# Performance work log

Hardware: AMD Instinct MI355X
Metric: run time of the kernel (lower is better)

The kernel has to match this reference:

```python
import jax, jax.numpy as jnp
import numpy as np
from jax import lax

THRESHOLDS = (0.25, 0.5, 0.75)
TAU = 100.0
NUM_CLASSES = 10
K = 32
RES_Z = 5.0
# each of the 16 binary logic gates is bilinear: g(a,b) = c0 + c1*a + c2*b + c3*a*b
GATE_COEF = jnp.array([
    [0, 0, 0, 0],   # 0: False
    [0, 0, 0, 1],   # 1: a AND b
    [0, 1, 0, -1],  # 2: a AND NOT b
    [0, 1, 0, 0],   # 3: a  (residual gate)
    [0, 0, 1, -1],  # 4: NOT a AND b
    [0, 0, 1, 0],   # 5: b
    [0, 1, 1, -2],  # 6: XOR
    [0, 1, 1, -1],  # 7: OR
    [1, -1, -1, 1], # 8: NOR
    [1, -1, -1, 2], # 9: XNOR
    [1, 0, -1, 0],  # 10: NOT b
    [1, 0, -1, 1],  # 11: a OR NOT b
    [1, -1, 0, 0],  # 12: NOT a
    [1, -1, 0, 1],  # 13: NOT a OR b
    [1, 0, 0, -1],  # 14: NAND
    [1, 0, 0, 0],   # 15: True
], dtype=jnp.float32)


def _gate_logits(key, shape):
    # residual init: pass-through gate (id 3) dominates
    w = 0.01 * jax.random.normal(key, shape, dtype=jnp.float32)
    return w.at[..., 3].add(RES_Z)


def _leaf_idx(rng, C, O, leaves=8, cpt=2, kk=9):
    # each tree uses cpt random input channels; each leaf picks one of them and a 3x3 position
    ch2 = rng.integers(0, C, size=(O, cpt))
    sel = rng.integers(0, cpt, size=(O, leaves))
    ch = np.take_along_axis(ch2, sel, axis=1)
    pos = rng.integers(0, kk, size=(O, leaves))
    return jnp.asarray(ch * kk + pos, dtype=jnp.int32)


def setup_inputs() -> dict:
    key = jax.random.key(0)
    ks = jax.random.split(key, 9)
    rng = np.random.default_rng(0)
    B = 128
    d = {"x": jax.random.uniform(ks[0], (B, 3, 32, 32), dtype=jnp.float32)}
    in_chs = [3 * len(THRESHOLDS), K, 4 * K, 16 * K]
    out_chs = [K, 4 * K, 16 * K, 32 * K]
    for i, (ci, co) in enumerate(zip(in_chs, out_chs)):
        d[f"c{i+1}_idx"] = _leaf_idx(rng, ci, co)
        d[f"c{i+1}_w"] = _gate_logits(ks[1 + i], (co, 7, 16))
    dims = [32 * K * 4, 1280 * K, 640 * K, 320 * K]
    for i in range(3):
        di, do = dims[i], dims[i + 1]
        d[f"l{i+1}_a"] = jnp.asarray(rng.integers(0, di, size=(do,)), dtype=jnp.int32)
        d[f"l{i+1}_b"] = jnp.asarray(rng.integers(0, di, size=(do,)), dtype=jnp.int32)
        d[f"l{i+1}_w"] = _gate_logits(ks[5 + i], (do, 16))
    return d


def _mix(logits):
    # softmax over 16 gates folded into 4 bilinear coefficients (fused gate mixture)
    return jax.nn.softmax(logits, axis=-1) @ GATE_COEF


def binarize(x):
    return jnp.concatenate([(x > t).astype(x.dtype) for t in THRESHOLDS], axis=1)


def tree_conv(x, leaf_idx, logits):
    # x: (B,C,H,W); leaf_idx: (O,8) into C*9 channel-major patch; logits: (O,7,16)
    B, C, H, W = x.shape
    xp = jnp.pad(x, ((0, 0), (0, 0), (1, 1), (1, 1)))
    patches = jnp.stack([xp[:, :, i:i + H, j:j + W] for i in range(3) for j in range(3)], axis=2)
    patches = patches.reshape(B, C * 9, H, W)
    vals = patches[:, leaf_idx]  # (B,O,8,H,W)
    m = _mix(logits)             # (O,7,4)
    node = 0
    for lvl in (4, 2, 1):
        a, b = vals[:, :, 0::2], vals[:, :, 1::2]
        w = m[:, node:node + lvl]  # (O,lvl,4)
        w0 = w[..., 0][None, :, :, None, None]
        w1 = w[..., 1][None, :, :, None, None]
        w2 = w[..., 2][None, :, :, None, None]
        w3 = w[..., 3][None, :, :, None, None]
        vals = w0 + w1 * a + w2 * b + w3 * (a * b)
        node += lvl
    return vals[:, :, 0]  # (B,O,H,W)


def or_pool(x):
    # OR of relaxed binary values == max pool 2x2/2
    return lax.reduce_window(x, -jnp.inf, lax.max, (1, 1, 2, 2), (1, 1, 2, 2), "VALID")


def logic_layer(x, a_idx, b_idx, logits):
    a = x[:, a_idx]  # (B,O)
    b = x[:, b_idx]
    w = _mix(logits)  # (O,4)
    return w[:, 0] + w[:, 1] * a + w[:, 2] * b + w[:, 3] * (a * b)


def group_sum(x):
    B = x.shape[0]
    return x.reshape(B, NUM_CLASSES, -1).sum(axis=-1) / TAU


def reference(x, c1_idx, c1_w, c2_idx, c2_w, c3_idx, c3_w, c4_idx, c4_w,
              l1_a, l1_b, l1_w, l2_a, l2_b, l2_w, l3_a, l3_b, l3_w):
    h = binarize(x)
    h = or_pool(tree_conv(h, c1_idx, c1_w))
    h = or_pool(tree_conv(h, c2_idx, c2_w))
    h = or_pool(tree_conv(h, c3_idx, c3_w))
    h = or_pool(tree_conv(h, c4_idx, c4_w))
    h = h.reshape(h.shape[0], -1)  # (B, 4096)
    h = logic_layer(h, l1_a, l1_b, l1_w)
    h = logic_layer(h, l2_a, l2_b, l2_w)
    h = logic_layer(h, l3_a, l3_b, l3_w)
    return group_sum(h)  # (B, 10)
```

## Files before the change

### kernel.cpp

```cpp
#include <hip/hip_runtime.h>

#define BATCH 128

__device__ __constant__ float GC[16][4] = {
  {0,0,0,0},{0,0,0,1},{0,1,0,-1},{0,1,0,0},
  {0,0,1,-1},{0,0,1,0},{0,1,1,-2},{0,1,1,-1},
  {1,-1,-1,1},{1,-1,-1,2},{1,0,-1,0},{1,0,-1,1},
  {1,-1,0,0},{1,-1,0,1},{1,0,0,-1},{1,0,0,0}};

struct MixArgs {
  const float* logits[7];
  float* out[7];
  int n[7];
};

__global__ __launch_bounds__(256) void mix_kernel(MixArgs args, int total) {
  int gid = blockIdx.x * 256 + threadIdx.x;
  if (gid >= total) return;
  int g = gid;
  int seg = 0;
  while (seg < 6 && g >= args.n[seg]) { g -= args.n[seg]; ++seg; }
  const float* lp = args.logits[seg] + (size_t)g * 16;
  float* op = args.out[seg] + (size_t)g * 4;

  float e[16];
  float s = 0.f;
  #pragma unroll
  for (int i = 0; i < 16; ++i) { e[i] = __expf(lp[i]); s += e[i]; }
  float inv = 1.0f / s;
  float w0 = 0.f, w1 = 0.f, w2 = 0.f, w3 = 0.f;
  #pragma unroll
  for (int i = 0; i < 16; ++i) {
    float p = e[i] * inv;
    w0 = fmaf(p, GC[i][0], w0);
    w1 = fmaf(p, GC[i][1], w1);
    w2 = fmaf(p, GC[i][2], w2);
    w3 = fmaf(p, GC[i][3], w3);
  }
  op[0] = w0; op[1] = w1; op[2] = w2; op[3] = w3;
}

__global__ __launch_bounds__(256) void transpose_x(
    const float* __restrict__ x, float* __restrict__ xt) {
  __shared__ float tile[64 * 129];
  int c    = blockIdx.x;
  int pix0 = blockIdx.y * 64;
  {
    int pix = threadIdx.x & 63;
    int b0  = threadIdx.x >> 6;
    #pragma unroll 4
    for (int i = 0; i < 32; ++i) {
      int b = b0 + i * 4;
      tile[pix * 129 + b] = x[((size_t)(b * 3 + c) * 1024) + pix0 + pix];
    }
  }
  __syncthreads();
  {
    int b     = threadIdx.x & 127;
    int pix0i = threadIdx.x >> 7;
    #pragma unroll 4
    for (int i = 0; i < 32; ++i) {
      int pix = pix0i + i * 2;
      xt[(size_t)(c * 1024 + pix0 + pix) * BATCH + b] = tile[pix * 129 + b];
    }
  }
}

__device__ __forceinline__ float2 gate2(float2 a, float2 b, float4 w) {
  float2 r;
  r.x = fmaf(w.w, a.x * b.x, fmaf(w.z, b.x, fmaf(w.y, a.x, w.x)));
  r.y = fmaf(w.w, a.y * b.y, fmaf(w.z, b.y, fmaf(w.y, a.y, w.x)));
  return r;
}

template <int C, int H, int W, int O, bool BIN>
__global__ __launch_bounds__(256) void tree_conv_pool_t(
    const float* __restrict__ in_t, const int* __restrict__ leaf_idx,
    const float* __restrict__ m, float* __restrict__ out_t) {
  constexpr int PH = H / 2, PW = W / 2, PIX = PH * PW;

  int wave = threadIdx.x >> 6;
  int b2   = threadIdx.x & 63;
  int q = blockIdx.x * 4 + wave;
  int o = q / PIX;
  int p = q - o * PIX;
  int ph = p / PW;
  int pw = p - ph * PW;

  int4 liA = ((const int4*)(leaf_idx + o * 8))[0];
  int4 liB = ((const int4*)(leaf_idx + o * 8))[1];
  int li[8] = {liA.x, liA.y, liA.z, liA.w, liB.x, liB.y, liB.z, liB.w};
  const float4* mw = (const float4*)(m + o * 28);

  float2 v[4][8];
  #pragma unroll
  for (int l = 0; l < 8; ++l) {
    int idx = li[l];
    int c = idx / 9;
    int k = idx - c * 9;
    int di = k / 3 - 1;
    int dj = (k % 3) - 1;
    int srcc;
    float th = 0.f;
    if (BIN) {
      int ti = c / 3;
      srcc = c - ti * 3;
      th = 0.25f * (float)(ti + 1);
    } else {
      srcc = c;
    }
    const float2* base =
        (const float2*)(in_t + (size_t)(srcc * H * W) * BATCH) + b2;
    #pragma unroll
    for (int pp = 0; pp < 4; ++pp) {
      int y = 2 * ph + (pp >> 1) + di;
      int x = 2 * pw + (pp & 1) + dj;
      float2 val = {0.f, 0.f};
      if ((unsigned)y < (unsigned)H && (unsigned)x < (unsigned)W) {
        val = base[(size_t)(y * W + x) * 64];
        if (BIN) {
          val.x = (val.x > th) ? 1.f : 0.f;
          val.y = (val.y > th) ? 1.f : 0.f;
        }
      }
      v[pp][l] = val;
    }
  }

  float4 w0 = mw[0], w1 = mw[1], w2 = mw[2], w3 = mw[3];
  float4 w4 = mw[4], w5 = mw[5], w6 = mw[6];
  float2 best = {-1e30f, -1e30f};
  #pragma unroll
  for (int pp = 0; pp < 4; ++pp) {
    float2 u0 = gate2(v[pp][0], v[pp][1], w0);
    float2 u1 = gate2(v[pp][2], v[pp][3], w1);
    float2 u2 = gate2(v[pp][4], v[pp][5], w2);
    float2 u3 = gate2(v[pp][6], v[pp][7], w3);
    float2 s0 = gate2(u0, u1, w4);
    float2 s1 = gate2(u2, u3, w5);
    float2 r  = gate2(s0, s1, w6);
    best.x = fmaxf(best.x, r.x);
    best.y = fmaxf(best.y, r.y);
  }

  ((float2*)(out_t + (size_t)q * BATCH))[b2] = best;
}

__global__ __launch_bounds__(256) void logic_layer_k(
    const float* __restrict__ in, const int* __restrict__ aidx,
    const int* __restrict__ bidx, const float* __restrict__ m,
    float* __restrict__ out) {
  int wave = threadIdx.x >> 6;
  int b2   = threadIdx.x & 63;
  int j0 = blockIdx.x * 16 + wave;
  #pragma unroll
  for (int it = 0; it < 4; ++it) {
    int j = j0 + it * 4;
    int ai = aidx[j];
    int bi = bidx[j];
    float4 w = ((const float4*)m)[j];
    float2 a  = ((const float2*)(in + (size_t)ai * BATCH))[b2];
    float2 bb = ((const float2*)(in + (size_t)bi * BATCH))[b2];
    ((float2*)(out + (size_t)j * BATCH))[b2] = gate2(a, bb, w);
  }
}

__global__ __launch_bounds__(64) void group_sum_partial(
    const float* __restrict__ in, float* __restrict__ part) {
  int cls   = blockIdx.x;
  int chunk = blockIdx.y;
  int b2    = threadIdx.x;
  const float2* p =
      (const float2*)(in + ((size_t)cls * 1024 + chunk * 128) * BATCH) + b2;
  float2 s = {0.f, 0.f};
  #pragma unroll 8
  for (int f = 0; f < 128; ++f) {
    float2 v = p[(size_t)f * 64];
    s.x += v.x; s.y += v.y;
  }
  ((float2*)(part + ((size_t)(cls * 8 + chunk)) * BATCH))[b2] = s;
}

__global__ __launch_bounds__(128) void group_sum_final(
    const float* __restrict__ part, float* __restrict__ out) {
  int t = blockIdx.x * 128 + threadIdx.x;
  int cls = t >> 7;
  int b   = t & 127;
  float s = 0.f;
  #pragma unroll
  for (int k = 0; k < 8; ++k) s += part[((size_t)cls * 8 + k) * BATCH + b];
  out[b * 10 + cls] = s * 0.01f;
}

extern "C" void kernel_launch(void* const* d_in, const int* in_sizes, int n_in,
                              void* d_out, int out_size, void* d_ws, size_t ws_size,
                              hipStream_t stream) {
  const float* x   = (const float*)d_in[0];
  const int*   c1i = (const int*)d_in[1];
  const float* c1w = (const float*)d_in[2];
  const int*   c2i = (const int*)d_in[3];
  const float* c2w = (const float*)d_in[4];
  const int*   c3i = (const int*)d_in[5];
  const float* c3w = (const float*)d_in[6];
  const int*   c4i = (const int*)d_in[7];
  const float* c4w = (const float*)d_in[8];
  const int*   l1a = (const int*)d_in[9];
  const int*   l1b = (const int*)d_in[10];
  const float* l1w = (const float*)d_in[11];
  const int*   l2a = (const int*)d_in[12];
  const int*   l2b = (const int*)d_in[13];
  const float* l2w = (const float*)d_in[14];
  const int*   l3a = (const int*)d_in[15];
  const int*   l3b = (const int*)d_in[16];
  const float* l3w = (const float*)d_in[17];

  float* ws = (float*)d_ws;

  float* mc1 = ws;
  float* mc2 = mc1 + 896;
  float* mc3 = mc2 + 3584;
  float* mc4 = mc3 + 14336;
  float* ml1 = mc4 + 28672;
  float* ml2 = ml1 + 163840;
  float* ml3 = ml2 + 81920;
  float* xt   = ml3 + 40960;
  float* actA = xt + 393216;
  float* actB = actA + 1048576;
  float* actC = actB + 1048576;
  float* actD = actC + 5242880;
  float* part = actD + 2621440;

  MixArgs ma;
  ma.logits[0] = c1w; ma.out[0] = mc1; ma.n[0] = 32 * 7;
  ma.logits[1] = c2w; ma.out[1] = mc2; ma.n[1] = 128 * 7;
  ma.logits[2] = c3w; ma.out[2] = mc3; ma.n[2] = 512 * 7;
  ma.logits[3] = c4w; ma.out[3] = mc4; ma.n[3] = 1024 * 7;
  ma.logits[4] = l1w; ma.out[4] = ml1; ma.n[4] = 40960;
  ma.logits[5] = l2w; ma.out[5] = ml2; ma.n[5] = 20480;
  ma.logits[6] = l3w; ma.out[6] = ml3; ma.n[6] = 10240;
  int total_gates = (32 + 128 + 512 + 1024) * 7 + 40960 + 20480 + 10240;
  mix_kernel<<<(total_gates + 255) / 256, 256, 0, stream>>>(ma, total_gates);

  transpose_x<<<dim3(3, 16), 256, 0, stream>>>(x, xt);

  tree_conv_pool_t<9, 32, 32, 32, true>
      <<<32 * 256 / 4, 256, 0, stream>>>(xt, c1i, mc1, actA);
  tree_conv_pool_t<32, 16, 16, 128, false>
      <<<128 * 64 / 4, 256, 0, stream>>>(actA, c2i, mc2, actB);
  tree_conv_pool_t<128, 8, 8, 512, false>
      <<<512 * 16 / 4, 256, 0, stream>>>(actB, c3i, mc3, actA);
  tree_conv_pool_t<512, 4, 4, 1024, false>
      <<<1024 * 4 / 4, 256, 0, stream>>>(actA, c4i, mc4, actB);

  logic_layer_k<<<40960 / 16, 256, 0, stream>>>(actB, l1a, l1b, ml1, actC);
  logic_layer_k<<<20480 / 16, 256, 0, stream>>>(actC, l2a, l2b, ml2, actD);
  logic_layer_k<<<10240 / 16, 256, 0, stream>>>(actD, l3a, l3b, ml3, actC);

  group_sum_partial<<<dim3(10, 8), 64, 0, stream>>>(actC, part);
  group_sum_final<<<10, 128, 0, stream>>>(part, (float*)d_out);
}
```

Measured before the change: 175.4 us.

## Fuse prep kernels, pre-binarize input, use packed FMA gates, fuse last layer with group sum

Mixing, input transpose and output zeroing now run in a single prep kernel, and the input is thresholded once into nine binarized channels instead of being compared inside the first conv. Gate evaluation uses inline-asm v_pk_fma_f32/v_pk_mul_f32. The conv kernel processes the pool window in two halves to reduce live registers, and uses readfirstlane to keep indices scalar. The final logic layer is fused with the group sum through atomicAdd, which removes two launches but makes the float summation order nondeterministic.

```diff
diff --git a/kernel.cpp b/kernel.cpp
--- a/kernel.cpp
+++ b/kernel.cpp
@@ -1,6 +1,9 @@
 #include <hip/hip_runtime.h>
 
 #define BATCH 128
+
+typedef float v2f __attribute__((ext_vector_type(2)));
+typedef float v4f __attribute__((ext_vector_type(4)));
 
 __device__ __constant__ float GC[16][4] = {
   {0,0,0,0},{0,0,0,1},{0,1,0,-1},{0,1,0,0},
@@ -8,21 +11,30 @@
   {1,-1,-1,1},{1,-1,-1,2},{1,0,-1,0},{1,0,-1,1},
   {1,-1,0,0},{1,-1,0,1},{1,0,0,-1},{1,0,0,0}};
 
-struct MixArgs {
-  const float* logits[7];
-  float* out[7];
-  int n[7];
-};
-
-__global__ __launch_bounds__(256) void mix_kernel(MixArgs args, int total) {
-  int gid = blockIdx.x * 256 + threadIdx.x;
-  if (gid >= total) return;
-  int g = gid;
-  int seg = 0;
-  while (seg < 6 && g >= args.n[seg]) { g -= args.n[seg]; ++seg; }
-  const float* lp = args.logits[seg] + (size_t)g * 16;
-  float* op = args.out[seg] + (size_t)g * 4;
-
+__device__ __forceinline__ v2f pk_mul(v2f a, v2f b) {
+  v2f d;
+  asm("v_pk_mul_f32 %0, %1, %2" : "=v"(d) : "v"(a), "v"(b));
+  return d;
+}
+__device__ __forceinline__ v2f max2(v2f a, v2f b) {
+  v2f d;
+  d.x = fmaxf(a.x, b.x);
+  d.y = fmaxf(a.y, b.y);
+  return d;
+}
+__device__ __forceinline__ v2f gate2pk(v2f a, v2f b, v2f w01, v2f w23) {
+  v2f t = pk_mul(a, b);
+  v2f d;
+  asm("v_pk_fma_f32 %0, %1, %2, %2 op_sel:[0,1,0] op_sel_hi:[1,1,0]"
+      : "=v"(d) : "v"(a), "v"(w01));
+  asm("v_pk_fma_f32 %0, %1, %2, %0 op_sel:[0,0,0] op_sel_hi:[1,0,1]"
+      : "+v"(d) : "v"(b), "v"(w23));
+  asm("v_pk_fma_f32 %0, %1, %2, %0 op_sel:[0,1,0] op_sel_hi:[1,1,1]"
+      : "+v"(d) : "v"(t), "v"(w23));
+  return d;
+}
+
+__device__ __forceinline__ void mix_one(const float* lp, float* op) {
   float e[16];
   float s = 0.f;
   #pragma unroll
@@ -40,113 +52,114 @@
   op[0] = w0; op[1] = w1; op[2] = w2; op[3] = w3;
 }
 
-__global__ __launch_bounds__(256) void transpose_x(
-    const float* __restrict__ x, float* __restrict__ xt) {
+struct PrepArgs {
+  const float* x;
+  const float* logits[7];
+  float* outm[7];
+  float* xtb;
+  float* out;
+};
+
+__global__ __launch_bounds__(256) void prep_k(PrepArgs A) {
   __shared__ float tile[64 * 129];
-  int c    = blockIdx.x;
-  int pix0 = blockIdx.y * 64;
-  {
-    int pix = threadIdx.x & 63;
-    int b0  = threadIdx.x >> 6;
-    #pragma unroll 4
-    for (int i = 0; i < 32; ++i) {
-      int b = b0 + i * 4;
-      tile[pix * 129 + b] = x[((size_t)(b * 3 + c) * 1024) + pix0 + pix];
-    }
-  }
-  __syncthreads();
-  {
-    int b     = threadIdx.x & 127;
-    int pix0i = threadIdx.x >> 7;
-    #pragma unroll 4
-    for (int i = 0; i < 32; ++i) {
-      int pix = pix0i + i * 2;
-      xt[(size_t)(c * 1024 + pix0 + pix) * BATCH + b] = tile[pix * 129 + b];
-    }
-  }
-}
-
-__device__ __forceinline__ float2 gate2(float2 a, float2 b, float4 w) {
-  float2 r;
-  r.x = fmaf(w.w, a.x * b.x, fmaf(w.z, b.x, fmaf(w.y, a.x, w.x)));
-  r.y = fmaf(w.w, a.y * b.y, fmaf(w.z, b.y, fmaf(w.y, a.y, w.x)));
-  return r;
-}
-
-template <int C, int H, int W, int O, bool BIN>
-__global__ __launch_bounds__(256) void tree_conv_pool_t(
-    const float* __restrict__ in_t, const int* __restrict__ leaf_idx,
+  int blk = blockIdx.x;
+  if (blk < 327) {
+    int gid = blk * 256 + threadIdx.x;
+    const int n[7] = {224, 896, 3584, 7168, 40960, 20480, 10240};
+    if (gid < 83552) {
+      int g = gid, seg = 0;
+      while (seg < 6 && g >= n[seg]) { g -= n[seg]; ++seg; }
+      mix_one(A.logits[seg] + (size_t)g * 16, A.outm[seg] + (size_t)g * 4);
+    }
+  } else if (blk < 327 + 144) {
+    int tb = blk - 327;
+    int c    = tb / 16;
+    int pix0 = (tb % 16) * 64;
+    int ti = c / 3, rgb = c - ti * 3;
+    float th = 0.25f * (float)(ti + 1);
+    {
+      int pix = threadIdx.x & 63;
+      int b0  = threadIdx.x >> 6;
+      #pragma unroll 4
+      for (int i = 0; i < 32; ++i) {
+        int b = b0 + i * 4;
+        float xv = A.x[(size_t)(b * 3 + rgb) * 1024 + pix0 + pix];
+        tile[pix * 129 + b] = (xv > th) ? 1.f : 0.f;
+      }
+    }
+    __syncthreads();
+    {
+      int b  = threadIdx.x & 127;
+      int p0 = threadIdx.x >> 7;
+      #pragma unroll 4
+      for (int i = 0; i < 32; ++i) {
+        int pix = p0 + i * 2;
+        A.xtb[(size_t)(c * 1024 + pix0 + pix) * BATCH + b] = tile[pix * 129 + b];
+      }
+    }
+  } else {
+    int t = threadIdx.x;
+    #pragma unroll
+    for (int i = 0; i < 5; ++i) A.out[t * 5 + i] = 0.f;
+  }
+}
+
+template <int H, int W>
+__global__ __launch_bounds__(256) void conv_t(
+    const float* __restrict__ in_t, const int* __restrict__ li_g,
     const float* __restrict__ m, float* __restrict__ out_t) {
-  constexpr int PH = H / 2, PW = W / 2, PIX = PH * PW;
-
+  constexpr int PH = H / 2, PWD = W / 2, PIX = PH * PWD;
   int wave = threadIdx.x >> 6;
   int b2   = threadIdx.x & 63;
-  int q = blockIdx.x * 4 + wave;
+  int q = __builtin_amdgcn_readfirstlane(blockIdx.x * 4 + wave);
   int o = q / PIX;
   int p = q - o * PIX;
-  int ph = p / PW;
-  int pw = p - ph * PW;
-
-  int4 liA = ((const int4*)(leaf_idx + o * 8))[0];
-  int4 liB = ((const int4*)(leaf_idx + o * 8))[1];
-  int li[8] = {liA.x, liA.y, liA.z, liA.w, liB.x, liB.y, liB.z, liB.w};
-  const float4* mw = (const float4*)(m + o * 28);
-
-  float2 v[4][8];
-  #pragma unroll
-  for (int l = 0; l < 8; ++l) {
-    int idx = li[l];
-    int c = idx / 9;
-    int k = idx - c * 9;
-    int di = k / 3 - 1;
-    int dj = (k % 3) - 1;
-    int srcc;
-    float th = 0.f;
-    if (BIN) {
-      int ti = c / 3;
-      srcc = c - ti * 3;
-      th = 0.25f * (float)(ti + 1);
-    } else {
-      srcc = c;
-    }
-    const float2* base =
-        (const float2*)(in_t + (size_t)(srcc * H * W) * BATCH) + b2;
+  int ph = p / PWD;
+  int pw = p - ph * PWD;
+
+  const int* li = li_g + o * 8;
+  const v4f* mv = (const v4f*)(m + o * 28);
+  v4f g0 = mv[0], g1 = mv[1], g2 = mv[2], g3 = mv[3];
+  v4f g4 = mv[4], g5 = mv[5], g6 = mv[6];
+
+  v2f best = {-1e30f, -1e30f};
+  #pragma unroll
+  for (int half = 0; half < 2; ++half) {
+    v2f v[2][8];
     #pragma unroll
-    for (int pp = 0; pp < 4; ++pp) {
-      int y = 2 * ph + (pp >> 1) + di;
-      int x = 2 * pw + (pp & 1) + dj;
-      float2 val = {0.f, 0.f};
-      if ((unsigned)y < (unsigned)H && (unsigned)x < (unsigned)W) {
-        val = base[(size_t)(y * W + x) * 64];
-        if (BIN) {
-          val.x = (val.x > th) ? 1.f : 0.f;
-          val.y = (val.y > th) ? 1.f : 0.f;
-        }
+    for (int l = 0; l < 8; ++l) {
+      int idx = li[l];
+      int c = idx / 9;
+      int k = idx - c * 9;
+      int di = k / 3 - 1;
+      int dj = (k - (k / 3) * 3) - 1;
+      const float* base = in_t + (size_t)(c * H * W) * BATCH;
+      int y = 2 * ph + half + di;
+      #pragma unroll
+      for (int pi = 0; pi < 2; ++pi) {
+        int x = 2 * pw + pi + dj;
+        v2f val = {0.f, 0.f};
+        if ((unsigned)y < (unsigned)H && (unsigned)x < (unsigned)W)
+          val = ((const v2f*)(base + (size_t)(y * W + x) * BATCH))[b2];
+        v[pi][l] = val;
       }
-      v[pp][l] = val;
-    }
-  }
-
-  float4 w0 = mw[0], w1 = mw[1], w2 = mw[2], w3 = mw[3];
-  float4 w4 = mw[4], w5 = mw[5], w6 = mw[6];
-  float2 best = {-1e30f, -1e30f};
-  #pragma unroll
-  for (int pp = 0; pp < 4; ++pp) {
-    float2 u0 = gate2(v[pp][0], v[pp][1], w0);
-    float2 u1 = gate2(v[pp][2], v[pp][3], w1);
-    float2 u2 = gate2(v[pp][4], v[pp][5], w2);
-    float2 u3 = gate2(v[pp][6], v[pp][7], w3);
-    float2 s0 = gate2(u0, u1, w4);
-    float2 s1 = gate2(u2, u3, w5);
-    float2 r  = gate2(s0, s1, w6);
-    best.x = fmaxf(best.x, r.x);
-    best.y = fmaxf(best.y, r.y);
-  }
-
-  ((float2*)(out_t + (size_t)q * BATCH))[b2] = best;
-}
-
-__global__ __launch_bounds__(256) void logic_layer_k(
+    }
+    #pragma unroll
+    for (int pi = 0; pi < 2; ++pi) {
+      v2f u0 = gate2pk(v[pi][0], v[pi][1], g0.xy, g0.zw);
+      v2f u1 = gate2pk(v[pi][2], v[pi][3], g1.xy, g1.zw);
+      v2f u2 = gate2pk(v[pi][4], v[pi][5], g2.xy, g2.zw);
+      v2f u3 = gate2pk(v[pi][6], v[pi][7], g3.xy, g3.zw);
+      v2f s0 = gate2pk(u0, u1, g4.xy, g4.zw);
+      v2f s1 = gate2pk(u2, u3, g5.xy, g5.zw);
+      v2f r  = gate2pk(s0, s1, g6.xy, g6.zw);
+      best = max2(best, r);
+    }
+  }
+  ((v2f*)(out_t + (size_t)q * BATCH))[b2] = best;
+}
+
+__global__ __launch_bounds__(256) void logic_k(
     const float* __restrict__ in, const int* __restrict__ aidx,
     const int* __restrict__ bidx, const float* __restrict__ m,
     float* __restrict__ out) {
@@ -155,41 +168,37 @@
   int j0 = blockIdx.x * 16 + wave;
   #pragma unroll
   for (int it = 0; it < 4; ++it) {
-    int j = j0 + it * 4;
+    int j = __builtin_amdgcn_readfirstlane(j0 + it * 4);
     int ai = aidx[j];
     int bi = bidx[j];
-    float4 w = ((const float4*)m)[j];
-    float2 a  = ((const float2*)(in + (size_t)ai * BATCH))[b2];
-    float2 bb = ((const float2*)(in + (size_t)bi * BATCH))[b2];
-    ((float2*)(out + (size_t)j * BATCH))[b2] = gate2(a, bb, w);
-  }
-}
-
-__global__ __launch_bounds__(64) void group_sum_partial(
-    const float* __restrict__ in, float* __restrict__ part) {
-  int cls   = blockIdx.x;
-  int chunk = blockIdx.y;
-  int b2    = threadIdx.x;
-  const float2* p =
-      (const float2*)(in + ((size_t)cls * 1024 + chunk * 128) * BATCH) + b2;
-  float2 s = {0.f, 0.f};
-  #pragma unroll 8
-  for (int f = 0; f < 128; ++f) {
-    float2 v = p[(size_t)f * 64];
-    s.x += v.x; s.y += v.y;
-  }
-  ((float2*)(part + ((size_t)(cls * 8 + chunk)) * BATCH))[b2] = s;
-}
-
-__global__ __launch_bounds__(128) void group_sum_final(
-    const float* __restrict__ part, float* __restrict__ out) {
-  int t = blockIdx.x * 128 + threadIdx.x;
-  int cls = t >> 7;
-  int b   = t & 127;
-  float s = 0.f;
-  #pragma unroll
-  for (int k = 0; k < 8; ++k) s += part[((size_t)cls * 8 + k) * BATCH + b];
-  out[b * 10 + cls] = s * 0.01f;
+    v4f w = ((const v4f*)m)[j];
+    v2f a = ((const v2f*)(in + (size_t)ai * BATCH))[b2];
+    v2f b = ((const v2f*)(in + (size_t)bi * BATCH))[b2];
+    ((v2f*)(out + (size_t)j * BATCH))[b2] = gate2pk(a, b, w.xy, w.zw);
+  }
+}
+
+__global__ __launch_bounds__(256) void logic3_gsum_k(
+    const float* __restrict__ in, const int* __restrict__ aidx,
+    const int* __restrict__ bidx, const float* __restrict__ m,
+    float* __restrict__ out) {
+  int wave = threadIdx.x >> 6;
+  int b2   = threadIdx.x & 63;
+  int j0 = __builtin_amdgcn_readfirstlane((blockIdx.x * 4 + wave) * 8);
+  int cls = j0 >> 10;
+  v2f s = {0.f, 0.f};
+  #pragma unroll
+  for (int it = 0; it < 8; ++it) {
+    int j = j0 + it;
+    int ai = aidx[j];
+    int bi = bidx[j];
+    v4f w = ((const v4f*)m)[j];
+    v2f a = ((const v2f*)(in + (size_t)ai * BATCH))[b2];
+    v2f b = ((const v2f*)(in + (size_t)bi * BATCH))[b2];
+    s += gate2pk(a, b, w.xy, w.zw);
+  }
+  atomicAdd(&out[(2 * b2) * 10 + cls], s.x * 0.01f);
+  atomicAdd(&out[(2 * b2 + 1) * 10 + cls], s.y * 0.01f);
 }
 
 extern "C" void kernel_launch(void* const* d_in, const int* in_sizes, int n_in,
@@ -215,7 +224,6 @@
   const float* l3w = (const float*)d_in[17];
 
   float* ws = (float*)d_ws;
-
   float* mc1 = ws;
   float* mc2 = mc1 + 896;
   float* mc3 = mc2 + 3584;
@@ -223,39 +231,34 @@
   float* ml1 = mc4 + 28672;
   float* ml2 = ml1 + 163840;
   float* ml3 = ml2 + 81920;
-  float* xt   = ml3 + 40960;
-  float* actA = xt + 393216;
-  float* actB = actA + 1048576;
-  float* actC = actB + 1048576;
-  float* actD = actC + 5242880;
-  float* part = actD + 2621440;
-
-  MixArgs ma;
-  ma.logits[0] = c1w; ma.out[0] = mc1; ma.n[0] = 32 * 7;
-  ma.logits[1] = c2w; ma.out[1] = mc2; ma.n[1] = 128 * 7;
-  ma.logits[2] = c3w; ma.out[2] = mc3; ma.n[2] = 512 * 7;
-  ma.logits[3] = c4w; ma.out[3] = mc4; ma.n[3] = 1024 * 7;
-  ma.logits[4] = l1w; ma.out[4] = ml1; ma.n[4] = 40960;
-  ma.logits[5] = l2w; ma.out[5] = ml2; ma.n[5] = 20480;
-  ma.logits[6] = l3w; ma.out[6] = ml3; ma.n[6] = 10240;
-  int total_gates = (32 + 128 + 512 + 1024) * 7 + 40960 + 20480 + 10240;
-  mix_kernel<<<(total_gates + 255) / 256, 256, 0, stream>>>(ma, total_gates);
-
-  transpose_x<<<dim3(3, 16), 256, 0, stream>>>(x, xt);
-
-  tree_conv_pool_t<9, 32, 32, 32, true>
-      <<<32 * 256 / 4, 256, 0, stream>>>(xt, c1i, mc1, actA);
-  tree_conv_pool_t<32, 16, 16, 128, false>
-      <<<128 * 64 / 4, 256, 0, stream>>>(actA, c2i, mc2, actB);
-  tree_conv_pool_t<128, 8, 8, 512, false>
-      <<<512 * 16 / 4, 256, 0, stream>>>(actB, c3i, mc3, actA);
-  tree_conv_pool_t<512, 4, 4, 1024, false>
-      <<<1024 * 4 / 4, 256, 0, stream>>>(actA, c4i, mc4, actB);
-
-  logic_layer_k<<<40960 / 16, 256, 0, stream>>>(actB, l1a, l1b, ml1, actC);
-  logic_layer_k<<<20480 / 16, 256, 0, stream>>>(actC, l2a, l2b, ml2, actD);
-  logic_layer_k<<<10240 / 16, 256, 0, stream>>>(actD, l3a, l3b, ml3, actC);
-
-  group_sum_partial<<<dim3(10, 8), 64, 0, stream>>>(actC, part);
-  group_sum_final<<<10, 128, 0, stream>>>(part, (float*)d_out);
-}
+  float* xtb = ml3 + 40960;
+  float* h1  = xtb + 1179648;
+  float* h2  = h1 + 1048576;
+  float* h3  = h2 + 1048576;
+  float* h4  = h3 + 1048576;
+  float* g1  = h4 + 524288;
+  float* g2  = g1 + 5242880;
+
+  PrepArgs A;
+  A.x = x;
+  A.logits[0] = c1w; A.outm[0] = mc1;
+  A.logits[1] = c2w; A.outm[1] = mc2;
+  A.logits[2] = c3w; A.outm[2] = mc3;
+  A.logits[3] = c4w; A.outm[3] = mc4;
+  A.logits[4] = l1w; A.outm[4] = ml1;
+  A.logits[5] = l2w; A.outm[5] = ml2;
+  A.logits[6] = l3w; A.outm[6] = ml3;
+  A.xtb = xtb;
+  A.out = (float*)d_out;
+  prep_k<<<472, 256, 0, stream>>>(A);
+
+  conv_t<32, 32><<<8192 / 4, 256, 0, stream>>>(xtb, c1i, mc1, h1);
+  conv_t<16, 16><<<8192 / 4, 256, 0, stream>>>(h1, c2i, mc2, h2);
+  conv_t<8, 8><<<8192 / 4, 256, 0, stream>>>(h2, c3i, mc3, h3);
+  conv_t<4, 4><<<4096 / 4, 256, 0, stream>>>(h3, c4i, mc4, h4);
+
+  logic_k<<<40960 / 16, 256, 0, stream>>>(h4, l1a, l1b, ml1, g1);
+  logic_k<<<20480 / 16, 256, 0, stream>>>(g1, l2a, l2b, ml2, g2);
+  logic3_gsum_k<<<10240 / 32, 256, 0, stream>>>(g2, l3a, l3b, ml3,
+                                                (float*)d_out);
+}
```

Measured after the change: 200.8 us. +14.5%, slower.
